# Optimization experiments

Measured on AMD Instinct MI355X. Metric: run time of the kernel, lower is better.

The kernel has to match this reference:

```python
import jax, jax.numpy as jnp
import numpy as np

N = 50000
E = 600000
HIDDEN = 128
HEADS = 4
HEAD_DIM = HIDDEN // HEADS
NEG_SLOPE = 0.2
LN_EPS = 1e-5


def setup_inputs() -> dict:
    key = jax.random.key(0)
    ks = jax.random.split(key, 16)
    s = 1.0 / np.sqrt(HIDDEN)
    inp = {
        "h": jax.random.normal(ks[0], (N, HIDDEN), dtype=jnp.float32),
        "src": jax.random.randint(ks[1], (E,), 0, N, dtype=jnp.int32),
        "dst": jax.random.randint(ks[2], (E,), 0, N, dtype=jnp.int32),
        # GATv2 params (share_weights=False, bias=True)
        "W_src": jax.random.normal(ks[3], (HIDDEN, HIDDEN), dtype=jnp.float32) * s,
        "b_src": jnp.zeros((HIDDEN,), dtype=jnp.float32),
        "W_dst": jax.random.normal(ks[4], (HIDDEN, HIDDEN), dtype=jnp.float32) * s,
        "b_dst": jnp.zeros((HIDDEN,), dtype=jnp.float32),
        "attn": jax.random.normal(ks[5], (HEADS, HEAD_DIM), dtype=jnp.float32) * s,
        # FFN params
        "W1": jax.random.normal(ks[6], (HIDDEN, 2 * HIDDEN), dtype=jnp.float32) * s,
        "bf1": jnp.zeros((2 * HIDDEN,), dtype=jnp.float32),
        "W2": jax.random.normal(ks[7], (2 * HIDDEN, HIDDEN), dtype=jnp.float32) * (1.0 / np.sqrt(2 * HIDDEN)),
        "bf2": jnp.zeros((HIDDEN,), dtype=jnp.float32),
        # LayerNorms
        "g1": jnp.ones((HIDDEN,), dtype=jnp.float32),
        "beta1": jnp.zeros((HIDDEN,), dtype=jnp.float32),
        "g2": jnp.ones((HIDDEN,), dtype=jnp.float32),
        "beta2": jnp.zeros((HIDDEN,), dtype=jnp.float32),
    }
    return inp


def _layernorm(x, g, b):
    mu = jnp.mean(x, axis=-1, keepdims=True)
    var = jnp.mean(jnp.square(x - mu), axis=-1, keepdims=True)
    return (x - mu) * jax.lax.rsqrt(var + LN_EPS) * g + b


def reference(h, src, dst, W_src, b_src, W_dst, b_dst, attn,
              W1, bf1, W2, bf2, g1, beta1, g2, beta2):
    # --- GATv2 attention (eval mode, dropouts are identity) ---
    fs = (h @ W_src + b_src).reshape(N, HEADS, HEAD_DIM)   # [N,H,D]
    fd = (h @ W_dst + b_dst).reshape(N, HEADS, HEAD_DIM)
    e = jax.nn.leaky_relu(fs[src] + fd[dst], NEG_SLOPE)    # [E,H,D]
    logits = jnp.einsum('ehd,hd->eh', e, attn)             # [E,H]
    # edge softmax over incoming edges of each dst node
    m = jax.ops.segment_max(logits, dst, num_segments=N)   # [N,H]
    m = jnp.where(jnp.isfinite(m), m, 0.0)                 # guard zero-in-degree
    a = jnp.exp(logits - m[dst])                           # [E,H]
    denom = jax.ops.segment_sum(a, dst, num_segments=N)    # [N,H]
    denom = jnp.where(denom == 0.0, 1.0, denom)
    alpha = a / denom[dst]                                 # [E,H]
    msg = fs[src] * alpha[:, :, None]                      # [E,H,D]
    rst = jax.ops.segment_sum(msg, dst, num_segments=N)    # [N,H,D]
    h_attn = rst.reshape(N, HIDDEN)
    # --- residual + LN, FFN + residual + LN ---
    h1 = _layernorm(h + h_attn, g1, beta1)
    ffn = jax.nn.gelu(h1 @ W1 + bf1, approximate=False) @ W2 + bf2
    out = _layernorm(h1 + ffn, g2, beta2)
    return out
```

## Files before the change

kernel.cpp:

```cpp
#include <hip/hip_runtime.h>
#include <math.h>

#define N_NODES 50000
#define N_EDGES 600000
#define HID 128
#define FFN_HID 256
#define NEG_SLOPE 0.2f
#define LN_EPS 1e-5f
#define BKT 64

#define GEMM_BLOCKS 1024
#define SCAT_BLOCKS 2344

typedef unsigned short u16;
typedef unsigned int u32;
typedef __attribute__((ext_vector_type(8))) short short8;
typedef __attribute__((ext_vector_type(4))) float floatx4;

__device__ __forceinline__ u16 f2bf(float x) {
    unsigned int u = __float_as_uint(x);
    unsigned int r = u + 0x7FFFu + ((u >> 16) & 1u);
    return (u16)(r >> 16);
}
__device__ __forceinline__ float bflo(u32 u) { return __uint_as_float(u << 16); }
__device__ __forceinline__ float bfhi(u32 u) { return __uint_as_float(u & 0xffff0000u); }
__device__ __forceinline__ u32 packbf(float lo, float hi) {
    return (u32)f2bf(lo) | ((u32)f2bf(hi) << 16);
}


__global__ void prep_zero(const float* __restrict__ Wsrc, const float* __restrict__ Wdst,
                          const float* __restrict__ W1, const float* __restrict__ W2,
                          u16* __restrict__ B1, u16* __restrict__ B2, u16* __restrict__ B3,
                          int* __restrict__ cursor) {
    int t = blockIdx.x * 256 + threadIdx.x;
    if (t < N_NODES) cursor[t] = 0;
    const float* W; u16* out; int K, Nc, noff;
    if (t < 16384)       { W = Wsrc; out = B1; K = 128; Nc = 128; noff = 0; }
    else if (t < 32768)  { W = Wdst; out = B1; K = 128; Nc = 128; noff = 128; t -= 16384; }
    else if (t < 65536)  { W = W1;   out = B2; K = 128; Nc = 256; noff = 0;   t -= 32768; }
    else if (t < 98304)  { W = W2;   out = B3; K = 256; Nc = 128; noff = 0;   t -= 65536; }
    else return;
    int n = t % Nc, k = t / Nc;
    int ng = noff + n;
    int ksteps = K >> 5;
    int frag = (ng >> 4) * ksteps + (k >> 5);
    int lane = ((k >> 3) & 3) * 16 + (ng & 15);
    int j = k & 7;
    out[((size_t)frag * 64 + lane) * 8 + j] = f2bf(W[(size_t)k * Nc + n]);
}


__global__ __launch_bounds__(256) void gemm_scatter(
    const float* __restrict__ h, const u16* __restrict__ Bsw,
    const float* __restrict__ bsrc, const float* __restrict__ bdst,
    u16* __restrict__ fsb, u16* __restrict__ fdb, u16* __restrict__ hb,
    const int* __restrict__ src, const int* __restrict__ dst,
    int* __restrict__ cursor, u16* __restrict__ ebkt)
{
    if (blockIdx.x >= GEMM_BLOCKS) {
        int e = (blockIdx.x - GEMM_BLOCKS) * 256 + threadIdx.x;
        if (e < N_EDGES) {
            int d = dst[e];
            int slot = atomicAdd(&cursor[d], 1);
            if (slot < BKT) ebkt[(size_t)d * BKT + slot] = (u16)src[e];
        }
        return;
    }
    int tid = threadIdx.x, wave = tid >> 6, lane = tid & 63;
    int lrow = lane & 15, lq = lane >> 4;
    short8 bfrag[4][4];
    #pragma unroll
    for (int nt = 0; nt < 4; nt++)
        #pragma unroll
        for (int ks = 0; ks < 4; ks++) {
            int frag = (wave * 4 + nt) * 4 + ks;
            bfrag[nt][ks] = *(const short8*)(Bsw + ((size_t)frag * 64 + lane) * 8);
        }
    float bias[4];
    #pragma unroll
    for (int nt = 0; nt < 4; nt++) {
        int cg = wave * 64 + nt * 16 + lrow;
        bias[nt] = (cg < HID) ? bsrc[cg] : bdst[cg - HID];
    }
    for (int mb = blockIdx.x; mb < N_NODES / 16; mb += GEMM_BLOCKS) {
        int m0 = mb * 16;
        const float* hrow = h + (size_t)(m0 + lrow) * HID;
        floatx4 acc[4];
        #pragma unroll
        for (int nt = 0; nt < 4; nt++) acc[nt] = {0.f, 0.f, 0.f, 0.f};
        #pragma unroll
        for (int ks = 0; ks < 4; ks++) {
            float4 va = *(const float4*)(hrow + ks * 32 + lq * 8);
            float4 vb = *(const float4*)(hrow + ks * 32 + lq * 8 + 4);
            short8 a;
            a[0] = (short)f2bf(va.x); a[1] = (short)f2bf(va.y);
            a[2] = (short)f2bf(va.z); a[3] = (short)f2bf(va.w);
            a[4] = (short)f2bf(vb.x); a[5] = (short)f2bf(vb.y);
            a[6] = (short)f2bf(vb.z); a[7] = (short)f2bf(vb.w);
            if (wave == 0)
                *(short8*)(hb + (size_t)(m0 + lrow) * HID + ks * 32 + lq * 8) = a;
            #pragma unroll
            for (int nt = 0; nt < 4; nt++)
                acc[nt] = __builtin_amdgcn_mfma_f32_16x16x32_bf16(a, bfrag[nt][ks], acc[nt], 0, 0, 0);
        }
        #pragma unroll
        for (int nt = 0; nt < 4; nt++) {
            int cg = wave * 64 + nt * 16 + lrow;
            u16* outp = (cg < HID) ? (fsb + cg) : (fdb + cg - HID);
            #pragma unroll
            for (int r = 0; r < 4; r++) {
                int row = m0 + lq * 4 + r;
                outp[(size_t)row * HID] = f2bf(acc[nt][r] + bias[nt]);
            }
        }
    }
}


__global__ __launch_bounds__(256) void aggregate_kernel(
    const u16* __restrict__ fsb, const u16* __restrict__ fdb,
    const u16* __restrict__ hb, const float* __restrict__ attn,
    const int* __restrict__ counts, const u16* __restrict__ ebkt,
    const float* __restrict__ g1, const float* __restrict__ beta1,
    u16* __restrict__ h1b)
{
    int wave = threadIdx.x >> 6, lane = threadIdx.x & 63;
    int node = blockIdx.x * 4 + wave;
    if (node >= N_NODES) return;
    int grp = lane >> 4, fl = lane & 15;
    int f = fl * 8;

    uint4 ud = *(const uint4*)&fdb[(size_t)node * HID + f];
    float fdv[8] = { bflo(ud.x), bfhi(ud.x), bflo(ud.y), bfhi(ud.y),
                     bflo(ud.z), bfhi(ud.z), bflo(ud.w), bfhi(ud.w) };
    float4 aA = *(const float4*)&attn[f];
    float4 aB = *(const float4*)&attn[f + 4];
    float c1[8] = { 0.6f * aA.x, 0.6f * aA.y, 0.6f * aA.z, 0.6f * aA.w,
                    0.6f * aB.x, 0.6f * aB.y, 0.6f * aB.z, 0.6f * aB.w };
    float c2[8] = { 0.4f * aA.x, 0.4f * aA.y, 0.4f * aA.z, 0.4f * aA.w,
                    0.4f * aB.x, 0.4f * aB.y, 0.4f * aB.z, 0.4f * aB.w };

    int cnt = counts[node]; cnt = cnt < BKT ? cnt : BKT;
    const u16* brow = ebkt + (size_t)node * BKT;
    float acc[8] = {0.f, 0.f, 0.f, 0.f, 0.f, 0.f, 0.f, 0.f};
    float lsum = 0.f;

    auto compute = [&](uint4 u) {
        float x[8] = { bflo(u.x), bfhi(u.x), bflo(u.y), bfhi(u.y),
                       bflo(u.z), bfhi(u.z), bflo(u.w), bfhi(u.w) };
        float p0 = 0.f, p1 = 0.f;
        #pragma unroll
        for (int i = 0; i < 4; i++) {
            float ei = x[i] + fdv[i];
            p0 = fmaf(c1[i], ei, p0);
            p0 = fmaf(c2[i], fabsf(ei), p0);
        }
        #pragma unroll
        for (int i = 4; i < 8; i++) {
            float ei = x[i] + fdv[i];
            p1 = fmaf(c1[i], ei, p1);
            p1 = fmaf(c2[i], fabsf(ei), p1);
        }
        float p = p0 + p1;
        p += __shfl_xor(p, 1); p += __shfl_xor(p, 2);
        float w = __expf(p);
        lsum += w;
        #pragma unroll
        for (int i = 0; i < 8; i++) acc[i] = fmaf(w, x[i], acc[i]);
    };

    int e = grp;
    for (; e + 4 < cnt; e += 8) {
        int sA = (int)brow[e], sB = (int)brow[e + 4];
        uint4 uA = *(const uint4*)&fsb[(size_t)sA * HID + f];
        uint4 uB = *(const uint4*)&fsb[(size_t)sB * HID + f];
        compute(uA);
        compute(uB);
    }
    if (e < cnt) {
        int s = (int)brow[e];
        compute(*(const uint4*)&fsb[(size_t)s * HID + f]);
    }

    #pragma unroll
    for (int i = 0; i < 8; i++) {
        acc[i] += __shfl_xor(acc[i], 16);
        acc[i] += __shfl_xor(acc[i], 32);
    }
    lsum += __shfl_xor(lsum, 16); lsum += __shfl_xor(lsum, 32);

    float inv = (lsum > 0.f) ? (1.0f / lsum) : 0.f;
    uint4 uh = *(const uint4*)&hb[(size_t)node * HID + f];
    float hx[8] = { bflo(uh.x), bfhi(uh.x), bflo(uh.y), bfhi(uh.y),
                    bflo(uh.z), bfhi(uh.z), bflo(uh.w), bfhi(uh.w) };
    float o[8], s1 = 0.f, s2 = 0.f;
    #pragma unroll
    for (int i = 0; i < 8; i++) {
        o[i] = hx[i] + acc[i] * inv;
        s1 += o[i]; s2 += o[i] * o[i];
    }
    s1 += __shfl_xor(s1, 1); s2 += __shfl_xor(s2, 1);
    s1 += __shfl_xor(s1, 2); s2 += __shfl_xor(s2, 2);
    s1 += __shfl_xor(s1, 4); s2 += __shfl_xor(s2, 4);
    s1 += __shfl_xor(s1, 8); s2 += __shfl_xor(s2, 8);
    float mu = s1 * (1.0f / HID);
    float var = s2 * (1.0f / HID) - mu * mu;
    float rs = rsqrtf(var + LN_EPS);
    if (grp == 0) {
        float4 gA = *(const float4*)&g1[f], gB = *(const float4*)&g1[f + 4];
        float4 bA = *(const float4*)&beta1[f], bB = *(const float4*)&beta1[f + 4];
        float q0 = (o[0] - mu) * rs * gA.x + bA.x, q1 = (o[1] - mu) * rs * gA.y + bA.y;
        float q2 = (o[2] - mu) * rs * gA.z + bA.z, q3 = (o[3] - mu) * rs * gA.w + bA.w;
        float q4 = (o[4] - mu) * rs * gB.x + bB.x, q5 = (o[5] - mu) * rs * gB.y + bB.y;
        float q6 = (o[6] - mu) * rs * gB.z + bB.z, q7 = (o[7] - mu) * rs * gB.w + bB.w;
        uint4 ob;
        ob.x = packbf(q0, q1); ob.y = packbf(q2, q3);
        ob.z = packbf(q4, q5); ob.w = packbf(q6, q7);
        *(uint4*)&h1b[(size_t)node * HID + f] = ob;
    }
}


#define TS_PAD 8

__device__ __forceinline__ float gelu_fast(float v) {
    float y = 0.7978845608f * (v + 0.044715f * v * v * v);
    y = fminf(fmaxf(y, -15.f), 15.f);
    float z = __expf(2.f * y);
    float th = (z - 1.f) / (z + 1.f);
    return 0.5f * v * (1.f + th);
}

__global__ __launch_bounds__(256) void ffn_fused(
    const u16* __restrict__ h1b, const u16* __restrict__ B2sw, const u16* __restrict__ B3sw,
    const float* __restrict__ bf1, const float* __restrict__ bf2,
    const float* __restrict__ g2, const float* __restrict__ beta2,
    float* __restrict__ out)
{
    __shared__ u16 ts[16][FFN_HID + TS_PAD];
    __shared__ float xs[16][HID];
    int tid = threadIdx.x, wave = tid >> 6, lane = tid & 63;
    int lrow = lane & 15, lq = lane >> 4;

    short8 b1f[4][4];
    #pragma unroll
    for (int nt = 0; nt < 4; nt++)
        #pragma unroll
        for (int ks = 0; ks < 4; ks++) {
            int frag = (wave * 4 + nt) * 4 + ks;
            b1f[nt][ks] = *(const short8*)(B2sw + ((size_t)frag * 64 + lane) * 8);
        }
    short8 b2f[2][8];
    #pragma unroll
    for (int nt = 0; nt < 2; nt++)
        #pragma unroll
        for (int ks = 0; ks < 8; ks++) {
            int frag = (wave * 2 + nt) * 8 + ks;
            b2f[nt][ks] = *(const short8*)(B3sw + ((size_t)frag * 64 + lane) * 8);
        }
    float bias1[4];
    #pragma unroll
    for (int nt = 0; nt < 4; nt++) bias1[nt] = bf1[wave * 64 + nt * 16 + lrow];
    float bias2[2];
    #pragma unroll
    for (int nt = 0; nt < 2; nt++) bias2[nt] = bf2[wave * 32 + nt * 16 + lrow];

    for (int mb = blockIdx.x; mb < N_NODES / 16; mb += gridDim.x) {
        int m0 = mb * 16;
        floatx4 acc1[4];
        #pragma unroll
        for (int nt = 0; nt < 4; nt++) acc1[nt] = {0.f, 0.f, 0.f, 0.f};
        #pragma unroll
        for (int ks = 0; ks < 4; ks++) {
            short8 a = *(const short8*)(h1b + (size_t)(m0 + lrow) * HID + ks * 32 + lq * 8);
            #pragma unroll
            for (int nt = 0; nt < 4; nt++)
                acc1[nt] = __builtin_amdgcn_mfma_f32_16x16x32_bf16(a, b1f[nt][ks], acc1[nt], 0, 0, 0);
        }
        #pragma unroll
        for (int nt = 0; nt < 4; nt++) {
            int cg = wave * 64 + nt * 16 + lrow;
            #pragma unroll
            for (int r = 0; r < 4; r++) {
                float v = acc1[nt][r] + bias1[nt];
                ts[lq * 4 + r][cg] = f2bf(gelu_fast(v));
            }
        }
        __syncthreads();
        floatx4 acc2[2];
        #pragma unroll
        for (int nt = 0; nt < 2; nt++) acc2[nt] = {0.f, 0.f, 0.f, 0.f};
        #pragma unroll
        for (int ks = 0; ks < 8; ks++) {
            short8 a = *(const short8*)&ts[lrow][ks * 32 + lq * 8];
            #pragma unroll
            for (int nt = 0; nt < 2; nt++)
                acc2[nt] = __builtin_amdgcn_mfma_f32_16x16x32_bf16(a, b2f[nt][ks], acc2[nt], 0, 0, 0);
        }
        #pragma unroll
        for (int nt = 0; nt < 2; nt++) {
            int cg = wave * 32 + nt * 16 + lrow;
            #pragma unroll
            for (int r = 0; r < 4; r++) {
                int row = m0 + lq * 4 + r;
                float resid = __uint_as_float(((u32)h1b[(size_t)row * HID + cg]) << 16);
                xs[lq * 4 + r][cg] = acc2[nt][r] + bias2[nt] + resid;
            }
        }
        __syncthreads();
        int row = tid >> 4, c0 = (tid & 15) * 8;
        float v[8];
        float s1 = 0.f, s2 = 0.f;
        #pragma unroll
        for (int i = 0; i < 8; i++) { v[i] = xs[row][c0 + i]; s1 += v[i]; s2 += v[i] * v[i]; }
        s1 += __shfl_xor(s1, 1); s2 += __shfl_xor(s2, 1);
        s1 += __shfl_xor(s1, 2); s2 += __shfl_xor(s2, 2);
        s1 += __shfl_xor(s1, 4); s2 += __shfl_xor(s2, 4);
        s1 += __shfl_xor(s1, 8); s2 += __shfl_xor(s2, 8);
        float mu = s1 * (1.0f / HID);
        float var = s2 * (1.0f / HID) - mu * mu;
        float rs = rsqrtf(var + LN_EPS);
        float o[8];
        #pragma unroll
        for (int i = 0; i < 8; i++) o[i] = (v[i] - mu) * rs * g2[c0 + i] + beta2[c0 + i];
        float* op = out + (size_t)(m0 + row) * HID + c0;
        *(float4*)(op)     = make_float4(o[0], o[1], o[2], o[3]);
        *(float4*)(op + 4) = make_float4(o[4], o[5], o[6], o[7]);
        __syncthreads();
    }
}


extern "C" void kernel_launch(void* const* d_in, const int* in_sizes, int n_in,
                              void* d_out, int out_size, void* d_ws, size_t ws_size,
                              hipStream_t stream)
{
    const float* h    = (const float*)d_in[0];
    const int*   src  = (const int*)d_in[1];
    const int*   dst  = (const int*)d_in[2];
    const float* Wsrc = (const float*)d_in[3];
    const float* bsrc = (const float*)d_in[4];
    const float* Wdst = (const float*)d_in[5];
    const float* bdst = (const float*)d_in[6];
    const float* attn = (const float*)d_in[7];
    const float* W1   = (const float*)d_in[8];
    const float* bf1  = (const float*)d_in[9];
    const float* W2   = (const float*)d_in[10];
    const float* bf2  = (const float*)d_in[11];
    const float* g1   = (const float*)d_in[12];
    const float* beta1= (const float*)d_in[13];
    const float* g2   = (const float*)d_in[14];
    const float* beta2= (const float*)d_in[15];
    float* out = (float*)d_out;

    u16* fsb = (u16*)d_ws;
    u16* fdb = fsb + (size_t)N_NODES * HID;
    u16* h1b = fdb + (size_t)N_NODES * HID;
    u16* hb  = h1b + (size_t)N_NODES * HID;
    u16* B1 = hb + (size_t)N_NODES * HID;
    u16* B2 = B1 + 32768;
    u16* B3 = B2 + 32768;
    int* cursor = (int*)(B3 + 32768);
    u16* ebkt   = (u16*)(cursor + N_NODES);

    prep_zero<<<384, 256, 0, stream>>>(Wsrc, Wdst, W1, W2, B1, B2, B3, cursor);
    gemm_scatter<<<GEMM_BLOCKS + SCAT_BLOCKS, 256, 0, stream>>>(
        h, B1, bsrc, bdst, fsb, fdb, hb, src, dst, cursor, ebkt);
    aggregate_kernel<<<(N_NODES + 3) / 4, 256, 0, stream>>>(fsb, fdb, hb, attn, cursor, ebkt, g1, beta1, h1b);
    ffn_fused<<<640, 256, 0, stream>>>(h1b, B2, B3, bf1, bf2, g2, beta2, out);
}
```

Measured before the change: 248.6 us.

## Move edge scatter into prep kernel and prefetch next tile in fs/fd GEMM

The edge bucketing moves out of the GEMM launch and into the weight-swizzle prep kernel, with each thread now handling four edges. The cursor array is zeroed with a memset instead of inside the prep kernel. The fs/fd GEMM becomes a standalone kernel that software-prefetches the next 16-row tile of h into registers while computing the current one, to hide global load latency. This adds a memset launch and extra register pressure, and the scatter no longer overlaps with the GEMM.

```diff
diff --git a/kernel.cpp b/kernel.cpp
--- a/kernel.cpp
+++ b/kernel.cpp
@@ -10,7 +10,9 @@
 #define BKT 64
 
 #define GEMM_BLOCKS 1024
-#define SCAT_BLOCKS 2344
+#define N_TILES (N_NODES / 16)
+#define SCAT_BLOCKS 586
+#define PREP_BLOCKS 384
 
 typedef unsigned short u16;
 typedef unsigned int u32;
@@ -29,12 +31,27 @@
 }
 
 
-__global__ void prep_zero(const float* __restrict__ Wsrc, const float* __restrict__ Wdst,
-                          const float* __restrict__ W1, const float* __restrict__ W2,
-                          u16* __restrict__ B1, u16* __restrict__ B2, u16* __restrict__ B3,
-                          int* __restrict__ cursor) {
-    int t = blockIdx.x * 256 + threadIdx.x;
-    if (t < N_NODES) cursor[t] = 0;
+__global__ void scatter_prep(const int* __restrict__ src, const int* __restrict__ dst,
+                             int* __restrict__ cursor, u16* __restrict__ ebkt,
+                             const float* __restrict__ Wsrc, const float* __restrict__ Wdst,
+                             const float* __restrict__ W1, const float* __restrict__ W2,
+                             u16* __restrict__ B1, u16* __restrict__ B2, u16* __restrict__ B3) {
+    int b = blockIdx.x;
+    if (b < SCAT_BLOCKS) {
+        int e0 = b * 1024 + threadIdx.x;
+        #pragma unroll
+        for (int i = 0; i < 4; i++) {
+            int e = e0 + i * 256;
+            if (e < N_EDGES) {
+                int d = dst[e];
+                int s = src[e];
+                int slot = atomicAdd(&cursor[d], 1);
+                if (slot < BKT) ebkt[(size_t)d * BKT + slot] = (u16)s;
+            }
+        }
+        return;
+    }
+    int t = (b - SCAT_BLOCKS) * 256 + threadIdx.x;
     const float* W; u16* out; int K, Nc, noff;
     if (t < 16384)       { W = Wsrc; out = B1; K = 128; Nc = 128; noff = 0; }
     else if (t < 32768)  { W = Wdst; out = B1; K = 128; Nc = 128; noff = 128; t -= 16384; }
@@ -51,22 +68,11 @@
 }
 
 
-__global__ __launch_bounds__(256) void gemm_scatter(
+__global__ __launch_bounds__(256) void gemm_fsfd_mfma(
     const float* __restrict__ h, const u16* __restrict__ Bsw,
     const float* __restrict__ bsrc, const float* __restrict__ bdst,
-    u16* __restrict__ fsb, u16* __restrict__ fdb, u16* __restrict__ hb,
-    const int* __restrict__ src, const int* __restrict__ dst,
-    int* __restrict__ cursor, u16* __restrict__ ebkt)
+    u16* __restrict__ fsb, u16* __restrict__ fdb, u16* __restrict__ hb)
 {
-    if (blockIdx.x >= GEMM_BLOCKS) {
-        int e = (blockIdx.x - GEMM_BLOCKS) * 256 + threadIdx.x;
-        if (e < N_EDGES) {
-            int d = dst[e];
-            int slot = atomicAdd(&cursor[d], 1);
-            if (slot < BKT) ebkt[(size_t)d * BKT + slot] = (u16)src[e];
-        }
-        return;
-    }
     int tid = threadIdx.x, wave = tid >> 6, lane = tid & 63;
     int lrow = lane & 15, lq = lane >> 4;
     short8 bfrag[4][4];
@@ -83,21 +89,40 @@
         int cg = wave * 64 + nt * 16 + lrow;
         bias[nt] = (cg < HID) ? bsrc[cg] : bdst[cg - HID];
     }
-    for (int mb = blockIdx.x; mb < N_NODES / 16; mb += GEMM_BLOCKS) {
+
+    float4 va[4], vb[4];
+    int mb = blockIdx.x;
+    {
+        const float* hrow = h + (size_t)(mb * 16 + lrow) * HID;
+        #pragma unroll
+        for (int ks = 0; ks < 4; ks++) {
+            va[ks] = *(const float4*)(hrow + ks * 32 + lq * 8);
+            vb[ks] = *(const float4*)(hrow + ks * 32 + lq * 8 + 4);
+        }
+    }
+    for (;;) {
+        int mn = mb + GEMM_BLOCKS;
+        bool more = (mn < N_TILES);
+        float4 nva[4], nvb[4];
+        if (more) {
+            const float* hrow = h + (size_t)(mn * 16 + lrow) * HID;
+            #pragma unroll
+            for (int ks = 0; ks < 4; ks++) {
+                nva[ks] = *(const float4*)(hrow + ks * 32 + lq * 8);
+                nvb[ks] = *(const float4*)(hrow + ks * 32 + lq * 8 + 4);
+            }
+        }
         int m0 = mb * 16;
-        const float* hrow = h + (size_t)(m0 + lrow) * HID;
         floatx4 acc[4];
         #pragma unroll
         for (int nt = 0; nt < 4; nt++) acc[nt] = {0.f, 0.f, 0.f, 0.f};
         #pragma unroll
         for (int ks = 0; ks < 4; ks++) {
-            float4 va = *(const float4*)(hrow + ks * 32 + lq * 8);
-            float4 vb = *(const float4*)(hrow + ks * 32 + lq * 8 + 4);
             short8 a;
-            a[0] = (short)f2bf(va.x); a[1] = (short)f2bf(va.y);
-            a[2] = (short)f2bf(va.z); a[3] = (short)f2bf(va.w);
-            a[4] = (short)f2bf(vb.x); a[5] = (short)f2bf(vb.y);
-            a[6] = (short)f2bf(vb.z); a[7] = (short)f2bf(vb.w);
+            a[0] = (short)f2bf(va[ks].x); a[1] = (short)f2bf(va[ks].y);
+            a[2] = (short)f2bf(va[ks].z); a[3] = (short)f2bf(va[ks].w);
+            a[4] = (short)f2bf(vb[ks].x); a[5] = (short)f2bf(vb[ks].y);
+            a[6] = (short)f2bf(vb[ks].z); a[7] = (short)f2bf(vb[ks].w);
             if (wave == 0)
                 *(short8*)(hb + (size_t)(m0 + lrow) * HID + ks * 32 + lq * 8) = a;
             #pragma unroll
@@ -114,6 +139,10 @@
                 outp[(size_t)row * HID] = f2bf(acc[nt][r] + bias[nt]);
             }
         }
+        if (!more) break;
+        #pragma unroll
+        for (int ks = 0; ks < 4; ks++) { va[ks] = nva[ks]; vb[ks] = nvb[ks]; }
+        mb = mn;
     }
 }
 
@@ -266,7 +295,7 @@
     #pragma unroll
     for (int nt = 0; nt < 2; nt++) bias2[nt] = bf2[wave * 32 + nt * 16 + lrow];
 
-    for (int mb = blockIdx.x; mb < N_NODES / 16; mb += gridDim.x) {
+    for (int mb = blockIdx.x; mb < N_TILES; mb += gridDim.x) {
         int m0 = mb * 16;
         floatx4 acc1[4];
         #pragma unroll
@@ -364,9 +393,10 @@
     int* cursor = (int*)(B3 + 32768);
     u16* ebkt   = (u16*)(cursor + N_NODES);
 
-    prep_zero<<<384, 256, 0, stream>>>(Wsrc, Wdst, W1, W2, B1, B2, B3, cursor);
-    gemm_scatter<<<GEMM_BLOCKS + SCAT_BLOCKS, 256, 0, stream>>>(
-        h, B1, bsrc, bdst, fsb, fdb, hb, src, dst, cursor, ebkt);
+    hipMemsetAsync(cursor, 0, N_NODES * sizeof(int), stream);
+    scatter_prep<<<SCAT_BLOCKS + PREP_BLOCKS, 256, 0, stream>>>(
+        src, dst, cursor, ebkt, Wsrc, Wdst, W1, W2, B1, B2, B3);
+    gemm_fsfd_mfma<<<GEMM_BLOCKS, 256, 0, stream>>>(h, B1, bsrc, bdst, fsb, fdb, hb);
     aggregate_kernel<<<(N_NODES + 3) / 4, 256, 0, stream>>>(fsb, fdb, hb, attn, cursor, ebkt, g1, beta1, h1b);
     ffn_fused<<<640, 256, 0, stream>>>(h1b, B2, B3, bf1, bf2, g2, beta2, out);
 }
```

Result: no change. 247.3 us (-0.5%).
